# Optimization experiments

Measured on AMD Instinct MI355X. Metric: run time of the kernel, lower is better.

The kernel has to match this reference:

```python
import jax, jax.numpy as jnp
import numpy as np

D_MODEL = 1024
NUM_HEADS = 16
D_K = D_MODEL // NUM_HEADS
EPS = 1e-6


def setup_inputs() -> dict:
    key = jax.random.key(0)
    ks = jax.random.split(key, 16)
    B, S = 2, 2048
    sc_in = 1.0 / np.sqrt(D_MODEL)
    sc_na = 1.0 / np.sqrt(D_K)
    inp = {
        "Q": jax.random.normal(ks[0], (B, S, D_MODEL), jnp.float32),
        "K": jax.random.normal(ks[1], (B, S, D_MODEL), jnp.float32),
        "V": jax.random.normal(ks[2], (B, S, D_MODEL), jnp.float32),
        "mask": jax.random.randint(ks[3], (1, 1, S, S), 0, 2, jnp.int32),
        # projection weights stored [in, out] (math-equivalent to torch Linear)
        "wq": jax.random.normal(ks[4], (D_MODEL, D_MODEL), jnp.float32) * sc_in,
        "bq": jnp.zeros((D_MODEL,), jnp.float32),
        "wk": jax.random.normal(ks[5], (D_MODEL, D_MODEL), jnp.float32) * sc_in,
        "bk": jnp.zeros((D_MODEL,), jnp.float32),
        "wv": jax.random.normal(ks[6], (D_MODEL, D_MODEL), jnp.float32) * sc_in,
        "bv": jnp.zeros((D_MODEL,), jnp.float32),
        "wo": jax.random.normal(ks[7], (D_MODEL, D_MODEL), jnp.float32) * sc_in,
        "bo": jnp.zeros((D_MODEL,), jnp.float32),
        # NeuralAttention score-fn params (per-head-dim transforms)
        "wnq": jax.random.normal(ks[8], (D_K, D_K), jnp.float32) * sc_na,
        "bnq": jnp.zeros((D_K,), jnp.float32),
        "wnk": jax.random.normal(ks[9], (D_K, D_K), jnp.float32) * sc_na,
        "bnk": jnp.zeros((D_K,), jnp.float32),
        "temperature": jnp.ones((NUM_HEADS, 1, 1), jnp.float32),
        "gamma": jnp.ones((D_MODEL,), jnp.float32),
    }
    return inp


def _split_heads(x):
    B, S, _ = x.shape
    return x.reshape(B, S, NUM_HEADS, D_K).transpose(0, 2, 1, 3)  # [B,H,S,dk]


def reference(Q, K, V, mask, wq, bq, wk, bk, wv, bv, wo, bo,
              wnq, bnq, wnk, bnk, temperature, gamma):
    B, S, _ = Q.shape
    q = _split_heads(Q @ wq + bq)  # [B,H,S,dk]
    k = _split_heads(K @ wk + bk)
    v = _split_heads(V @ wv + bv)
    # NeuralAttention: nonlinear per-token feature maps, then contraction
    qf = jnp.tanh(q @ wnq + bnq)
    kf = jnp.tanh(k @ wnk + bnk)
    scores = jnp.einsum('bhqd,bhkd->bhqk', qf, kf) / jnp.sqrt(jnp.float32(D_K))
    scores = scores / temperature  # [H,1,1] broadcasts over [B,H,S,S]
    scores = jnp.where(mask == 0, jnp.float32(-1e9), scores)
    attn = jax.nn.softmax(scores, axis=-1)
    ctx = jnp.einsum('bhqk,bhkd->bhqd', attn, v)
    out = ctx.transpose(0, 2, 1, 3).reshape(B, S, D_MODEL) @ wo + bo
    # RMSNorm
    rms = jax.lax.rsqrt(jnp.mean(out * out, axis=-1, keepdims=True) + EPS)
    return out * rms * gamma
```

## Files before the change

kernel.cpp:

```cpp
#include <hip/hip_runtime.h>
#include <hip/hip_bf16.h>
#include <math.h>

#define S_LEN 2048
#define BATCH 2
#define NH 16
#define DK 64
#define DM 1024
#define BS (BATCH * S_LEN)
#define BHS (BATCH * NH * S_LEN)
#define TRP 72
#define PSTR 72

using bf16x8  = __attribute__((ext_vector_type(8))) __bf16;
using floatx4 = __attribute__((ext_vector_type(4))) float;
using ushort4v = __attribute__((ext_vector_type(4))) unsigned short;

extern "C" __device__ float __ocml_exp2_f32(float);

__device__ __forceinline__ unsigned short f2bf(float f) {
    union { float f; unsigned u; } v; v.f = f;
    unsigned r = v.u + 0x7fffu + ((v.u >> 16) & 1u);
    return (unsigned short)(r >> 16);
}

__device__ __forceinline__ unsigned cvt_pk_bf16(float a, float b) {
    unsigned r;
    asm("v_cvt_pk_bf16_f32 %0, %1, %2" : "=v"(r) : "v"(a), "v"(b));
    return r;
}

__device__ __forceinline__ float fast_tanh(float x) {
    float e = __ocml_exp2_f32(x * 2.8853900817779268f);
    return 1.0f - 2.0f / (e + 1.0f);
}

__device__ __forceinline__ void gl2lds16(const void* g, void* l) {
    __builtin_amdgcn_global_load_lds(
        (__attribute__((address_space(1))) void*)(uintptr_t)g,
        (__attribute__((address_space(3))) void*)(uintptr_t)l,
        16, 0, 0);
}

__global__ void k_convert(const float* __restrict__ q, const float* __restrict__ k,
                          const float* __restrict__ v,
                          unsigned short* __restrict__ qb, unsigned short* __restrict__ kb,
                          unsigned short* __restrict__ vb) {
    const int N4 = BS * DM / 4;
    int i = blockIdx.x * 256 + threadIdx.x;
    int which = i / N4;
    int off = i - which * N4;
    const floatx4* src = (const floatx4*)(which == 0 ? q : which == 1 ? k : v);
    unsigned short* dst = which == 0 ? qb : which == 1 ? kb : vb;
    floatx4 x = src[off];
    ushort4v o;
    unsigned p01 = cvt_pk_bf16(x[0], x[1]);
    unsigned p23 = cvt_pk_bf16(x[2], x[3]);
    o[0] = (unsigned short)p01; o[1] = (unsigned short)(p01 >> 16);
    o[2] = (unsigned short)p23; o[3] = (unsigned short)(p23 >> 16);
    ((ushort4v*)dst)[off] = o;
}

__global__ void k_transpose(const float* s0, const float* s1, const float* s2, const float* s3,
                            unsigned short* d0, unsigned short* d1, unsigned short* d2,
                            unsigned short* d3, int n) {
    int z = blockIdx.z;
    const float* src = z == 0 ? s0 : z == 1 ? s1 : z == 2 ? s2 : s3;
    unsigned short* dst = z == 0 ? d0 : z == 1 ? d1 : z == 2 ? d2 : d3;
    __shared__ unsigned short tile[32][33];
    int tx = threadIdx.x & 31, ty = threadIdx.x >> 5;
#pragma unroll
    for (int i = 0; i < 4; i++) {
        int y = blockIdx.y * 32 + i * 8 + ty;
        tile[i * 8 + ty][tx] = f2bf(src[(size_t)y * n + blockIdx.x * 32 + tx]);
    }
    __syncthreads();
#pragma unroll
    for (int i = 0; i < 4; i++) {
        int r = blockIdx.x * 32 + i * 8 + ty;
        dst[(size_t)r * n + blockIdx.y * 32 + tx] = tile[tx][i * 8 + ty];
    }
}

__global__ void k_maskpack(const int* __restrict__ mask, unsigned int* __restrict__ mb) {
    int t = blockIdx.x * 256 + threadIdx.x;
    int row = t >> 6, w = t & 63;
    const int* p = mask + (size_t)row * S_LEN + w * 32;
    unsigned bits = 0;
#pragma unroll
    for (int i = 0; i < 32; i++) bits |= (p[i] != 0 ? 1u : 0u) << i;
    mb[t] = bits;
}

__global__ __launch_bounds__(256) void k_gemm_qkv(
    const unsigned short* __restrict__ Qb, const unsigned short* __restrict__ Kb,
    const unsigned short* __restrict__ Vb,
    const unsigned short* __restrict__ Wqt, const unsigned short* __restrict__ Wkt,
    const unsigned short* __restrict__ Wvt,
    const float* __restrict__ bq, const float* __restrict__ bk, const float* __restrict__ bv,
    const unsigned short* __restrict__ wnqt, const unsigned short* __restrict__ wnkt,
    const float* __restrict__ bnq, const float* __restrict__ bnk,
    const float* __restrict__ temp,
    unsigned short* __restrict__ qfb, unsigned short* __restrict__ kfrag,
    unsigned short* __restrict__ vfrag) {
    const int K = DM;
    int z = blockIdx.z;
    const unsigned short* A  = z == 0 ? Qb  : z == 1 ? Kb  : Vb;
    const unsigned short* Wt = z == 0 ? Wqt : z == 1 ? Wkt : Wvt;
    const float* bias        = z == 0 ? bq  : z == 1 ? bk  : bv;
    int m0 = blockIdx.y * 128, n0 = blockIdx.x * 128;
    __shared__ unsigned short As[128 * 32];
    __shared__ unsigned short Bs[128 * 32];
    __shared__ unsigned short Tr[4][32 * TRP];
    int tid = threadIdx.x;
    int lane = tid & 63, wid = tid >> 6;
    int wy = wid >> 1, wx = wid & 1;
    int l16 = lane & 15, quad = lane >> 4;

    floatx4 acc[4][4] = {};

    for (int kt = 0; kt < K / 32; kt++) {
        int kk = kt * 32;
#pragma unroll
        for (int i = 0; i < 2; i++) {
            int c = i * 256 + tid;
            int row = c >> 2, seg = c & 3;
            gl2lds16(A + (size_t)(m0 + row) * K + kk + seg * 8, &As[c * 8]);
            gl2lds16(Wt + (size_t)(n0 + row) * K + kk + seg * 8, &Bs[c * 8]);
        }
        __syncthreads();
        bf16x8 af[4], bf[4];
#pragma unroll
        for (int mi = 0; mi < 4; mi++)
            af[mi] = *(const bf16x8*)&As[(wy * 64 + mi * 16 + l16) * 32 + quad * 8];
#pragma unroll
        for (int ni = 0; ni < 4; ni++)
            bf[ni] = *(const bf16x8*)&Bs[(wx * 64 + ni * 16 + l16) * 32 + quad * 8];
#pragma unroll
        for (int mi = 0; mi < 4; mi++)
#pragma unroll
            for (int ni = 0; ni < 4; ni++)
                acc[mi][ni] = __builtin_amdgcn_mfma_f32_16x16x32_bf16(af[mi], bf[ni], acc[mi][ni], 0, 0, 0);
        __syncthreads();
    }

    float bvv[4];
#pragma unroll
    for (int ni = 0; ni < 4; ni++) bvv[ni] = bias[n0 + wx * 64 + ni * 16 + l16];
    int head = (n0 + wx * 64) >> 6;
    int mbase = m0 + wy * 64;
    int b = mbase >> 11;
    int bh = b * NH + head;
    unsigned short* tw = &Tr[wid][0];

    if (z == 2) {
        int kt2 = (mbase & (S_LEN - 1)) >> 6;
        size_t tilebase = ((size_t)bh * 32 + kt2) * 4096;
#pragma unroll
        for (int hh = 0; hh < 2; hh++) {
#pragma unroll
            for (int ni2 = 0; ni2 < 2; ni2++) {
                int ni = hh * 2 + ni2;
#pragma unroll
                for (int mi = 0; mi < 4; mi++) {
                    unsigned p01 = cvt_pk_bf16(acc[mi][ni][0] + bvv[ni], acc[mi][ni][1] + bvv[ni]);
                    unsigned p23 = cvt_pk_bf16(acc[mi][ni][2] + bvv[ni], acc[mi][ni][3] + bvv[ni]);
                    int ad = (ni2 * 16 + l16) * TRP + mi * 16 + quad * 4;
                    *(unsigned*)&tw[ad] = p01;
                    *(unsigned*)&tw[ad + 2] = p23;
                }
            }
#pragma unroll
            for (int c = 0; c < 4; c++) {
                int ad = ((c >> 1) * 16 + l16) * TRP + (c & 1) * 32 + quad * 8;
                bf16x8 vv = *(const bf16x8*)&tw[ad];
                *(bf16x8*)&vfrag[tilebase + (size_t)(4 * hh + c) * 512 + lane * 8] = vv;
            }
        }
    } else {
        const unsigned short* wn = z == 0 ? wnqt : wnkt;
        const float* bn = z == 0 ? bnq : bnk;
        float sc = z == 0 ? 1.4426950408889634f / (8.0f * temp[head]) : 1.0f;
        bf16x8 wf[4][2];
        float bnv[4];
#pragma unroll
        for (int ni = 0; ni < 4; ni++) {
            bnv[ni] = bn[ni * 16 + l16];
#pragma unroll
            for (int ks = 0; ks < 2; ks++)
                wf[ni][ks] = *(const bf16x8*)(wn + (size_t)(ni * 16 + l16) * DK + ks * 32 + quad * 8);
        }
        size_t rowbase = (size_t)((size_t)bh * S_LEN + (mbase & (S_LEN - 1))) * DK;
        int kt2 = (mbase & (S_LEN - 1)) >> 6;
        size_t tb = ((size_t)bh * 32 + kt2) * 4096;
#pragma unroll
        for (int hh = 0; hh < 2; hh++) {
#pragma unroll
            for (int mi2 = 0; mi2 < 2; mi2++) {
                int mi = hh * 2 + mi2;
#pragma unroll
                for (int ni = 0; ni < 4; ni++) {
                    unsigned p01 = cvt_pk_bf16(acc[mi][ni][0] + bvv[ni], acc[mi][ni][1] + bvv[ni]);
                    unsigned p23 = cvt_pk_bf16(acc[mi][ni][2] + bvv[ni], acc[mi][ni][3] + bvv[ni]);
                    int ad = (mi2 * 16 + quad * 4) * TRP + ni * 16 + l16;
                    tw[ad] = (unsigned short)p01;
                    tw[ad + TRP] = (unsigned short)(p01 >> 16);
                    tw[ad + 2 * TRP] = (unsigned short)p23;
                    tw[ad + 3 * TRP] = (unsigned short)(p23 >> 16);
                }
            }
            floatx4 facc[2][4] = {};
#pragma unroll
            for (int mg = 0; mg < 2; mg++) {
                bf16x8 af2[2];
#pragma unroll
                for (int ks = 0; ks < 2; ks++)
                    af2[ks] = *(const bf16x8*)&tw[(mg * 16 + l16) * TRP + ks * 32 + quad * 8];
#pragma unroll
                for (int ni = 0; ni < 4; ni++) {
                    facc[mg][ni] = __builtin_amdgcn_mfma_f32_16x16x32_bf16(af2[0], wf[ni][0], facc[mg][ni], 0, 0, 0);
                    facc[mg][ni] = __builtin_amdgcn_mfma_f32_16x16x32_bf16(af2[1], wf[ni][1], facc[mg][ni], 0, 0, 0);
                }
            }
#pragma unroll
            for (int mg = 0; mg < 2; mg++) {
#pragma unroll
                for (int ni = 0; ni < 4; ni++) {
                    float t0 = fast_tanh(facc[mg][ni][0] + bnv[ni]) * sc;
                    float t1 = fast_tanh(facc[mg][ni][1] + bnv[ni]) * sc;
                    float t2 = fast_tanh(facc[mg][ni][2] + bnv[ni]) * sc;
                    float t3 = fast_tanh(facc[mg][ni][3] + bnv[ni]) * sc;
                    unsigned p01 = cvt_pk_bf16(t0, t1);
                    unsigned p23 = cvt_pk_bf16(t2, t3);
                    int ad = (mg * 16 + quad * 4) * TRP + ni * 16 + l16;
                    tw[ad] = (unsigned short)p01;
                    tw[ad + TRP] = (unsigned short)(p01 >> 16);
                    tw[ad + 2 * TRP] = (unsigned short)p23;
                    tw[ad + 3 * TRP] = (unsigned short)(p23 >> 16);
                }
            }
            if (z == 0) {
#pragma unroll
                for (int c = 0; c < 4; c++) {
                    int g = c * 64 + lane;
                    int ml = g >> 3, dc = g & 7;
                    bf16x8 vv = *(const bf16x8*)&tw[ml * TRP + dc * 8];
                    *(bf16x8*)&qfb[rowbase + (size_t)(hh * 32 + ml) * DK + dc * 8] = vv;
                }
            } else {
#pragma unroll
                for (int c = 0; c < 4; c++) {
                    int ad = ((c >> 1) * 16 + l16) * TRP + (c & 1) * 32 + quad * 8;
                    bf16x8 vv = *(const bf16x8*)&tw[ad];
                    *(bf16x8*)&kfrag[tb + (size_t)(hh * 4 + c) * 512 + lane * 8] = vv;
                }
            }
        }
    }
}

__global__ __launch_bounds__(256) void k_gemm_out(const unsigned short* __restrict__ A,
                                                  const unsigned short* __restrict__ Wt,
                                                  const float* __restrict__ bias,
                                                  float* __restrict__ out_f32) {
    const int K = DM;
    int m0 = blockIdx.y * 128, n0 = blockIdx.x * 128;
    __shared__ unsigned short As[128 * 32];
    __shared__ unsigned short Bs[128 * 32];
    int tid = threadIdx.x;
    int lane = tid & 63, wid = tid >> 6;
    int wy = wid >> 1, wx = wid & 1;
    int l16 = lane & 15, quad = lane >> 4;

    floatx4 acc[4][4] = {};

    for (int kt = 0; kt < K / 32; kt++) {
        int kk = kt * 32;
#pragma unroll
        for (int i = 0; i < 2; i++) {
            int c = i * 256 + tid;
            int row = c >> 2, seg = c & 3;
            gl2lds16(A + (size_t)(m0 + row) * K + kk + seg * 8, &As[c * 8]);
            gl2lds16(Wt + (size_t)(n0 + row) * K + kk + seg * 8, &Bs[c * 8]);
        }
        __syncthreads();
        bf16x8 af[4], bf[4];
#pragma unroll
        for (int mi = 0; mi < 4; mi++)
            af[mi] = *(const bf16x8*)&As[(wy * 64 + mi * 16 + l16) * 32 + quad * 8];
#pragma unroll
        for (int ni = 0; ni < 4; ni++)
            bf[ni] = *(const bf16x8*)&Bs[(wx * 64 + ni * 16 + l16) * 32 + quad * 8];
#pragma unroll
        for (int mi = 0; mi < 4; mi++)
#pragma unroll
            for (int ni = 0; ni < 4; ni++)
                acc[mi][ni] = __builtin_amdgcn_mfma_f32_16x16x32_bf16(af[mi], bf[ni], acc[mi][ni], 0, 0, 0);
        __syncthreads();
    }

#pragma unroll
    for (int mi = 0; mi < 4; mi++) {
#pragma unroll
        for (int ni = 0; ni < 4; ni++) {
            int col = n0 + wx * 64 + ni * 16 + l16;
            float bvv = bias[col];
#pragma unroll
            for (int r = 0; r < 4; r++) {
                int row = m0 + wy * 64 + mi * 16 + quad * 4 + r;
                out_f32[(size_t)row * DM + col] = acc[mi][ni][r] + bvv;
            }
        }
    }
}

__global__ __launch_bounds__(256, 2) void k_attn(const unsigned short* __restrict__ qf,
                                                 const unsigned short* __restrict__ kfr,
                                                 const unsigned short* __restrict__ vfr,
                                                 const unsigned long long* __restrict__ mb64,
                                                 unsigned short* __restrict__ ctx) {
    int tid = threadIdx.x, lane = tid & 63, wid = tid >> 6;
    int l16 = lane & 15, quad = lane >> 4;
    int bh = blockIdx.y;
    int b = bh >> 4, h = bh & 15;
    int q0 = blockIdx.x * 128 + wid * 32;

    const unsigned short* qfb = qf + (size_t)bh * S_LEN * DK;
    const unsigned short* kbase = kfr + (size_t)bh * 32 * 4096;
    const unsigned short* vbase = vfr + (size_t)bh * 32 * 4096;

    __shared__ unsigned short Kbuf[2][4096];
    __shared__ unsigned short Plds[4][32 * PSTR];
    unsigned short* myP = Plds[wid];

    bf16x8 bq[2][2];
#pragma unroll
    for (int g = 0; g < 2; g++)
#pragma unroll
        for (int ks = 0; ks < 2; ks++)
            bq[g][ks] = *(const bf16x8*)(qfb + (size_t)(q0 + g * 16 + l16) * DK + ks * 32 + quad * 8);

    gl2lds16(kbase + tid * 8, &Kbuf[0][tid * 8]);
    gl2lds16(kbase + 2048 + tid * 8, &Kbuf[0][2048 + tid * 8]);

    floatx4 oacc[2][4] = {};
    float lrow[2] = {0.f, 0.f};
    const unsigned long long* mq0 = mb64 + (size_t)(q0 + l16) * 32;
    const unsigned long long* mq1 = mb64 + (size_t)(q0 + 16 + l16) * 32;

    for (int kt = 0; kt < S_LEN / 64; kt++) {
        __syncthreads();
        int nb = (kt + 1) & 1;
        const unsigned short* kn = kbase + (size_t)((kt + 1) & 31) * 4096;
        gl2lds16(kn + tid * 8, &Kbuf[nb][tid * 8]);
        gl2lds16(kn + 2048 + tid * 8, &Kbuf[nb][2048 + tid * 8]);
        const unsigned short* vt = vbase + (size_t)kt * 4096 + lane * 8;
        bf16x8 vf[8];
#pragma unroll
        for (int i = 0; i < 8; i++) vf[i] = *(const bf16x8*)(vt + i * 512);
        unsigned long long mw[2] = {mq0[kt], mq1[kt]};
        const unsigned short* kb = &Kbuf[kt & 1][lane * 8];
        bf16x8 kf8[8];
#pragma unroll
        for (int i = 0; i < 8; i++) kf8[i] = *(const bf16x8*)(kb + i * 512);
#pragma unroll
        for (int g = 0; g < 2; g++) {
            unsigned short* pw = myP + (g * 16 + l16) * PSTR;
#pragma unroll
            for (int kbk = 0; kbk < 4; kbk++) {
                floatx4 s = {};
                s = __builtin_amdgcn_mfma_f32_16x16x32_bf16(kf8[kbk * 2], bq[g][0], s, 0, 0, 0);
                s = __builtin_amdgcn_mfma_f32_16x16x32_bf16(kf8[kbk * 2 + 1], bq[g][1], s, 0, 0, 0);
                unsigned w = (unsigned)(mw[g] >> (kbk * 16 + quad * 4));
                float p0 = __ocml_exp2_f32((w & 1u) ? s[0] : -23.0f);
                float p1 = __ocml_exp2_f32((w & 2u) ? s[1] : -23.0f);
                float p2 = __ocml_exp2_f32((w & 4u) ? s[2] : -23.0f);
                float p3 = __ocml_exp2_f32((w & 8u) ? s[3] : -23.0f);
                lrow[g] += (p0 + p1) + (p2 + p3);
                *(unsigned*)&pw[kbk * 16 + quad * 4] = cvt_pk_bf16(p0, p1);
                *(unsigned*)&pw[kbk * 16 + quad * 4 + 2] = cvt_pk_bf16(p2, p3);
            }
            bf16x8 pa0 = *(const bf16x8*)&myP[(g * 16 + l16) * PSTR + quad * 8];
            bf16x8 pa1 = *(const bf16x8*)&myP[(g * 16 + l16) * PSTR + 32 + quad * 8];
#pragma unroll
            for (int ni = 0; ni < 4; ni++) {
                oacc[g][ni] = __builtin_amdgcn_mfma_f32_16x16x32_bf16(pa0, vf[ni * 2], oacc[g][ni], 0, 0, 0);
                oacc[g][ni] = __builtin_amdgcn_mfma_f32_16x16x32_bf16(pa1, vf[ni * 2 + 1], oacc[g][ni], 0, 0, 0);
            }
        }
    }
#pragma unroll
    for (int g = 0; g < 2; g++) {
        float lr = lrow[g];
        lr += __shfl_xor(lr, 16);
        lr += __shfl_xor(lr, 32);
        float inv[4];
#pragma unroll
        for (int r = 0; r < 4; r++) inv[r] = 1.0f / __shfl(lr, quad * 4 + r, 16);
#pragma unroll
        for (int ni = 0; ni < 4; ni++) {
            int d = ni * 16 + l16;
#pragma unroll
            for (int r = 0; r < 4; r++) {
                int s = q0 + g * 16 + quad * 4 + r;
                ctx[(size_t)(b * S_LEN + s) * DM + h * DK + d] = f2bf(oacc[g][ni][r] * inv[r]);
            }
        }
    }
}

__global__ __launch_bounds__(256) void k_rmsnorm(const float* __restrict__ x,
                                                 const float* __restrict__ gamma,
                                                 float* __restrict__ out) {
    int row = blockIdx.x, tid = threadIdx.x;
    const floatx4* xr = (const floatx4*)(x + (size_t)row * DM);
    floatx4 v = xr[tid];
    float ss = v[0] * v[0] + v[1] * v[1] + v[2] * v[2] + v[3] * v[3];
#pragma unroll
    for (int off = 1; off < 64; off <<= 1) ss += __shfl_xor(ss, off);
    __shared__ float red[4];
    int lane = tid & 63, wid = tid >> 6;
    if (lane == 0) red[wid] = ss;
    __syncthreads();
    float tot = red[0] + red[1] + red[2] + red[3];
    float rms = rsqrtf(tot * (1.0f / DM) + 1e-6f);
    floatx4 g = ((const floatx4*)gamma)[tid];
    floatx4 o;
    o[0] = v[0] * rms * g[0];
    o[1] = v[1] * rms * g[1];
    o[2] = v[2] * rms * g[2];
    o[3] = v[3] * rms * g[3];
    ((floatx4*)(out + (size_t)row * DM))[tid] = o;
}

extern "C" void kernel_launch(void* const* d_in, const int* in_sizes, int n_in,
                              void* d_out, int out_size, void* d_ws, size_t ws_size,
                              hipStream_t stream) {
    const float* Q = (const float*)d_in[0];
    const float* K = (const float*)d_in[1];
    const float* V = (const float*)d_in[2];
    const int* mask = (const int*)d_in[3];
    const float* wq = (const float*)d_in[4];
    const float* bq = (const float*)d_in[5];
    const float* wk = (const float*)d_in[6];
    const float* bk = (const float*)d_in[7];
    const float* wv = (const float*)d_in[8];
    const float* bv = (const float*)d_in[9];
    const float* wo = (const float*)d_in[10];
    const float* bo = (const float*)d_in[11];
    const float* wnq = (const float*)d_in[12];
    const float* bnq = (const float*)d_in[13];
    const float* wnk = (const float*)d_in[14];
    const float* bnk = (const float*)d_in[15];
    const float* temp = (const float*)d_in[16];
    const float* gamma = (const float*)d_in[17];

    char* w = (char*)d_ws;
    size_t o = 0;
    auto alloc = [&](size_t bytes) {
        char* p = w + o;
        o += (bytes + 255) & ~(size_t)255;
        return p;
    };
    unsigned short* Qb = (unsigned short*)alloc((size_t)BS * DM * 2);
    unsigned short* Kb = (unsigned short*)alloc((size_t)BS * DM * 2);
    unsigned short* Vb = (unsigned short*)alloc((size_t)BS * DM * 2);
    unsigned short* Wqt = (unsigned short*)alloc((size_t)DM * DM * 2);
    unsigned short* Wkt = (unsigned short*)alloc((size_t)DM * DM * 2);
    unsigned short* Wvt = (unsigned short*)alloc((size_t)DM * DM * 2);
    unsigned short* Wot = (unsigned short*)alloc((size_t)DM * DM * 2);
    unsigned short* wnqt = (unsigned short*)alloc((size_t)DK * DK * 2);
    unsigned short* wnkt = (unsigned short*)alloc((size_t)DK * DK * 2);
    unsigned short* vfrag = (unsigned short*)alloc((size_t)BHS * DK * 2);
    unsigned short* qfb = (unsigned short*)alloc((size_t)BHS * DK * 2);
    unsigned short* kfrag = (unsigned short*)alloc((size_t)BHS * DK * 2);
    unsigned int* mb = (unsigned int*)alloc((size_t)S_LEN * (S_LEN / 32) * 4);
    unsigned short* ctx = (unsigned short*)alloc((size_t)BS * DM * 2);
    float* outt = (float*)alloc((size_t)BS * DM * 4);

    k_convert<<<dim3(3 * BS * DM / 4 / 256), 256, 0, stream>>>(Q, K, V, Qb, Kb, Vb);
    k_transpose<<<dim3(32, 32, 4), 256, 0, stream>>>(wq, wk, wv, wo, Wqt, Wkt, Wvt, Wot, DM);
    k_transpose<<<dim3(2, 2, 2), 256, 0, stream>>>(wnq, wnk, wnq, wnq, wnqt, wnkt, wnqt, wnqt, DK);
    k_maskpack<<<dim3(S_LEN * 64 / 256), 256, 0, stream>>>(mask, mb);

    k_gemm_qkv<<<dim3(8, 32, 3), 256, 0, stream>>>(Qb, Kb, Vb, Wqt, Wkt, Wvt,
                                                   bq, bk, bv, wnqt, wnkt, bnq, bnk, temp,
                                                   qfb, kfrag, vfrag);

    k_attn<<<dim3(S_LEN / 128, BATCH * NH), 256, 0, stream>>>(
        qfb, kfrag, vfrag, (const unsigned long long*)mb, ctx);

    k_gemm_out<<<dim3(8, 32), 256, 0, stream>>>(ctx, Wot, bo, outt);
    k_rmsnorm<<<dim3(BS), 256, 0, stream>>>(outt, gamma, (float*)d_out);
}
```

Before: 303.3 us.

## Split attention over key range, combine partials, and shrink output GEMM tiles

Result: slower. 325.8 us (+7.4%).

```diff
diff --git a/kernel.cpp b/kernel.cpp
--- a/kernel.cpp
+++ b/kernel.cpp
@@ -264,35 +264,33 @@
                                                   const float* __restrict__ bias,
                                                   float* __restrict__ out_f32) {
     const int K = DM;
-    int m0 = blockIdx.y * 128, n0 = blockIdx.x * 128;
+    int m0 = blockIdx.y * 128, n0 = blockIdx.x * 64;
     __shared__ unsigned short As[128 * 32];
-    __shared__ unsigned short Bs[128 * 32];
+    __shared__ unsigned short Bs[64 * 32];
     int tid = threadIdx.x;
     int lane = tid & 63, wid = tid >> 6;
-    int wy = wid >> 1, wx = wid & 1;
     int l16 = lane & 15, quad = lane >> 4;
 
-    floatx4 acc[4][4] = {};
+    floatx4 acc[2][4] = {};
 
     for (int kt = 0; kt < K / 32; kt++) {
         int kk = kt * 32;
 #pragma unroll
         for (int i = 0; i < 2; i++) {
             int c = i * 256 + tid;
-            int row = c >> 2, seg = c & 3;
-            gl2lds16(A + (size_t)(m0 + row) * K + kk + seg * 8, &As[c * 8]);
-            gl2lds16(Wt + (size_t)(n0 + row) * K + kk + seg * 8, &Bs[c * 8]);
-        }
+            gl2lds16(A + (size_t)(m0 + (c >> 2)) * K + kk + (c & 3) * 8, &As[c * 8]);
+        }
+        gl2lds16(Wt + (size_t)(n0 + (tid >> 2)) * K + kk + (tid & 3) * 8, &Bs[tid * 8]);
         __syncthreads();
-        bf16x8 af[4], bf[4];
-#pragma unroll
-        for (int mi = 0; mi < 4; mi++)
-            af[mi] = *(const bf16x8*)&As[(wy * 64 + mi * 16 + l16) * 32 + quad * 8];
+        bf16x8 af[2], bf[4];
+#pragma unroll
+        for (int mi = 0; mi < 2; mi++)
+            af[mi] = *(const bf16x8*)&As[(wid * 32 + mi * 16 + l16) * 32 + quad * 8];
 #pragma unroll
         for (int ni = 0; ni < 4; ni++)
-            bf[ni] = *(const bf16x8*)&Bs[(wx * 64 + ni * 16 + l16) * 32 + quad * 8];
-#pragma unroll
-        for (int mi = 0; mi < 4; mi++)
+            bf[ni] = *(const bf16x8*)&Bs[(ni * 16 + l16) * 32 + quad * 8];
+#pragma unroll
+        for (int mi = 0; mi < 2; mi++)
 #pragma unroll
             for (int ni = 0; ni < 4; ni++)
                 acc[mi][ni] = __builtin_amdgcn_mfma_f32_16x16x32_bf16(af[mi], bf[ni], acc[mi][ni], 0, 0, 0);
@@ -300,30 +298,32 @@
     }
 
 #pragma unroll
-    for (int mi = 0; mi < 4; mi++) {
+    for (int mi = 0; mi < 2; mi++) {
 #pragma unroll
         for (int ni = 0; ni < 4; ni++) {
-            int col = n0 + wx * 64 + ni * 16 + l16;
+            int col = n0 + ni * 16 + l16;
             float bvv = bias[col];
 #pragma unroll
             for (int r = 0; r < 4; r++) {
-                int row = m0 + wy * 64 + mi * 16 + quad * 4 + r;
+                int row = m0 + wid * 32 + mi * 16 + quad * 4 + r;
                 out_f32[(size_t)row * DM + col] = acc[mi][ni][r] + bvv;
             }
         }
     }
 }
 
-__global__ __launch_bounds__(256, 2) void k_attn(const unsigned short* __restrict__ qf,
+__global__ __launch_bounds__(256, 4) void k_attn(const unsigned short* __restrict__ qf,
                                                  const unsigned short* __restrict__ kfr,
                                                  const unsigned short* __restrict__ vfr,
                                                  const unsigned long long* __restrict__ mb64,
-                                                 unsigned short* __restrict__ ctx) {
+                                                 float* __restrict__ Opart,
+                                                 float* __restrict__ Lpart) {
     int tid = threadIdx.x, lane = tid & 63, wid = tid >> 6;
     int l16 = lane & 15, quad = lane >> 4;
     int bh = blockIdx.y;
-    int b = bh >> 4, h = bh & 15;
+    int z = blockIdx.z;
     int q0 = blockIdx.x * 128 + wid * 32;
+    int kt0 = z * 16;
 
     const unsigned short* qfb = qf + (size_t)bh * S_LEN * DK;
     const unsigned short* kbase = kfr + (size_t)bh * 32 * 4096;
@@ -333,6 +333,11 @@
     __shared__ unsigned short Plds[4][32 * PSTR];
     unsigned short* myP = Plds[wid];
 
+    union { bf16x8 v; unsigned short u[8]; } one_u;
+#pragma unroll
+    for (int j = 0; j < 8; j++) one_u.u[j] = 0x3F80;
+    bf16x8 ones = one_u.v;
+
     bf16x8 bq[2][2];
 #pragma unroll
     for (int g = 0; g < 2; g++)
@@ -340,18 +345,19 @@
         for (int ks = 0; ks < 2; ks++)
             bq[g][ks] = *(const bf16x8*)(qfb + (size_t)(q0 + g * 16 + l16) * DK + ks * 32 + quad * 8);
 
-    gl2lds16(kbase + tid * 8, &Kbuf[0][tid * 8]);
-    gl2lds16(kbase + 2048 + tid * 8, &Kbuf[0][2048 + tid * 8]);
+    gl2lds16(kbase + (size_t)kt0 * 4096 + tid * 8, &Kbuf[0][tid * 8]);
+    gl2lds16(kbase + (size_t)kt0 * 4096 + 2048 + tid * 8, &Kbuf[0][2048 + tid * 8]);
 
     floatx4 oacc[2][4] = {};
-    float lrow[2] = {0.f, 0.f};
+    floatx4 lacc[2] = {};
     const unsigned long long* mq0 = mb64 + (size_t)(q0 + l16) * 32;
     const unsigned long long* mq1 = mb64 + (size_t)(q0 + 16 + l16) * 32;
 
-    for (int kt = 0; kt < S_LEN / 64; kt++) {
+    for (int lk = 0; lk < 16; lk++) {
+        int kt = kt0 + lk;
         __syncthreads();
-        int nb = (kt + 1) & 1;
-        const unsigned short* kn = kbase + (size_t)((kt + 1) & 31) * 4096;
+        int nb = (lk + 1) & 1;
+        const unsigned short* kn = kbase + (size_t)(kt0 + ((lk + 1) & 15)) * 4096;
         gl2lds16(kn + tid * 8, &Kbuf[nb][tid * 8]);
         gl2lds16(kn + 2048 + tid * 8, &Kbuf[nb][2048 + tid * 8]);
         const unsigned short* vt = vbase + (size_t)kt * 4096 + lane * 8;
@@ -359,7 +365,7 @@
 #pragma unroll
         for (int i = 0; i < 8; i++) vf[i] = *(const bf16x8*)(vt + i * 512);
         unsigned long long mw[2] = {mq0[kt], mq1[kt]};
-        const unsigned short* kb = &Kbuf[kt & 1][lane * 8];
+        const unsigned short* kb = &Kbuf[lk & 1][lane * 8];
         bf16x8 kf8[8];
 #pragma unroll
         for (int i = 0; i < 8; i++) kf8[i] = *(const bf16x8*)(kb + i * 512);
@@ -376,12 +382,13 @@
                 float p1 = __ocml_exp2_f32((w & 2u) ? s[1] : -23.0f);
                 float p2 = __ocml_exp2_f32((w & 4u) ? s[2] : -23.0f);
                 float p3 = __ocml_exp2_f32((w & 8u) ? s[3] : -23.0f);
-                lrow[g] += (p0 + p1) + (p2 + p3);
                 *(unsigned*)&pw[kbk * 16 + quad * 4] = cvt_pk_bf16(p0, p1);
                 *(unsigned*)&pw[kbk * 16 + quad * 4 + 2] = cvt_pk_bf16(p2, p3);
             }
             bf16x8 pa0 = *(const bf16x8*)&myP[(g * 16 + l16) * PSTR + quad * 8];
             bf16x8 pa1 = *(const bf16x8*)&myP[(g * 16 + l16) * PSTR + 32 + quad * 8];
+            lacc[g] = __builtin_amdgcn_mfma_f32_16x16x32_bf16(pa0, ones, lacc[g], 0, 0, 0);
+            lacc[g] = __builtin_amdgcn_mfma_f32_16x16x32_bf16(pa1, ones, lacc[g], 0, 0, 0);
 #pragma unroll
             for (int ni = 0; ni < 4; ni++) {
                 oacc[g][ni] = __builtin_amdgcn_mfma_f32_16x16x32_bf16(pa0, vf[ni * 2], oacc[g][ni], 0, 0, 0);
@@ -389,24 +396,42 @@
             }
         }
     }
+    size_t obase = ((size_t)z * BHS + (size_t)bh * S_LEN) * DK;
+    size_t lbase = (size_t)z * BHS + (size_t)bh * S_LEN;
 #pragma unroll
     for (int g = 0; g < 2; g++) {
-        float lr = lrow[g];
-        lr += __shfl_xor(lr, 16);
-        lr += __shfl_xor(lr, 32);
-        float inv[4];
-#pragma unroll
-        for (int r = 0; r < 4; r++) inv[r] = 1.0f / __shfl(lr, quad * 4 + r, 16);
+        if (l16 == 0) {
+#pragma unroll
+            for (int r = 0; r < 4; r++)
+                Lpart[lbase + q0 + g * 16 + quad * 4 + r] = lacc[g][r];
+        }
 #pragma unroll
         for (int ni = 0; ni < 4; ni++) {
-            int d = ni * 16 + l16;
-#pragma unroll
-            for (int r = 0; r < 4; r++) {
-                int s = q0 + g * 16 + quad * 4 + r;
-                ctx[(size_t)(b * S_LEN + s) * DM + h * DK + d] = f2bf(oacc[g][ni][r] * inv[r]);
-            }
-        }
-    }
+#pragma unroll
+            for (int r = 0; r < 4; r++)
+                Opart[obase + (size_t)(q0 + g * 16 + quad * 4 + r) * DK + ni * 16 + l16] = oacc[g][ni][r];
+        }
+    }
+}
+
+__global__ __launch_bounds__(256) void k_combine(const float* __restrict__ O,
+                                                 const float* __restrict__ L,
+                                                 unsigned short* __restrict__ ctx) {
+    int gid = blockIdx.x * 256 + threadIdx.x;
+    size_t flat = (size_t)gid * 4;
+    int row = gid >> 4;
+    int d0 = (gid & 15) * 4;
+    floatx4 o0 = *(const floatx4*)&O[flat];
+    floatx4 o1 = *(const floatx4*)&O[(size_t)BHS * DK + flat];
+    float ri = 1.0f / (L[row] + L[BHS + row]);
+    int bh = row >> 11, s = row & (S_LEN - 1);
+    int b = bh >> 4, h = bh & 15;
+    unsigned p01 = cvt_pk_bf16((o0[0] + o1[0]) * ri, (o0[1] + o1[1]) * ri);
+    unsigned p23 = cvt_pk_bf16((o0[2] + o1[2]) * ri, (o0[3] + o1[3]) * ri);
+    ushort4v o;
+    o[0] = (unsigned short)p01; o[1] = (unsigned short)(p01 >> 16);
+    o[2] = (unsigned short)p23; o[3] = (unsigned short)(p23 >> 16);
+    *(ushort4v*)&ctx[((size_t)(b * S_LEN + s)) * DM + h * DK + d0] = o;
 }
 
 __global__ __launch_bounds__(256) void k_rmsnorm(const float* __restrict__ x,
@@ -477,6 +502,8 @@
     unsigned int* mb = (unsigned int*)alloc((size_t)S_LEN * (S_LEN / 32) * 4);
     unsigned short* ctx = (unsigned short*)alloc((size_t)BS * DM * 2);
     float* outt = (float*)alloc((size_t)BS * DM * 4);
+    float* Opart = (float*)alloc((size_t)2 * BHS * DK * 4);
+    float* Lpart = (float*)alloc((size_t)2 * BHS * 4);
 
     k_convert<<<dim3(3 * BS * DM / 4 / 256), 256, 0, stream>>>(Q, K, V, Qb, Kb, Vb);
     k_transpose<<<dim3(32, 32, 4), 256, 0, stream>>>(wq, wk, wv, wo, Wqt, Wkt, Wvt, Wot, DM);
@@ -487,9 +514,11 @@
                                                    bq, bk, bv, wnqt, wnkt, bnq, bnk, temp,
                                                    qfb, kfrag, vfrag);
 
-    k_attn<<<dim3(S_LEN / 128, BATCH * NH), 256, 0, stream>>>(
-        qfb, kfrag, vfrag, (const unsigned long long*)mb, ctx);
-
-    k_gemm_out<<<dim3(8, 32), 256, 0, stream>>>(ctx, Wot, bo, outt);
+    k_attn<<<dim3(S_LEN / 128, BATCH * NH, 2), 256, 0, stream>>>(
+        qfb, kfrag, vfrag, (const unsigned long long*)mb, Opart, Lpart);
+
+    k_combine<<<dim3(BHS * DK / 4 / 256), 256, 0, stream>>>(Opart, Lpart, ctx);
+
+    k_gemm_out<<<dim3(16, 32), 256, 0, stream>>>(ctx, Wot, bo, outt);
     k_rmsnorm<<<dim3(BS), 256, 0, stream>>>(outt, gamma, (float*)d_out);
 }
```

## Shrink attention and output-GEMM tiles for more blocks; MFMA row sums

Applied to the files above, without the earlier changes.

New measurement: 298.7 us. About the same (-1.5%).

```diff
diff --git a/kernel.cpp b/kernel.cpp
--- a/kernel.cpp
+++ b/kernel.cpp
@@ -264,35 +264,33 @@
                                                   const float* __restrict__ bias,
                                                   float* __restrict__ out_f32) {
     const int K = DM;
-    int m0 = blockIdx.y * 128, n0 = blockIdx.x * 128;
+    int m0 = blockIdx.y * 128, n0 = blockIdx.x * 64;
     __shared__ unsigned short As[128 * 32];
-    __shared__ unsigned short Bs[128 * 32];
+    __shared__ unsigned short Bs[64 * 32];
     int tid = threadIdx.x;
     int lane = tid & 63, wid = tid >> 6;
-    int wy = wid >> 1, wx = wid & 1;
     int l16 = lane & 15, quad = lane >> 4;
 
-    floatx4 acc[4][4] = {};
+    floatx4 acc[2][4] = {};
 
     for (int kt = 0; kt < K / 32; kt++) {
         int kk = kt * 32;
 #pragma unroll
         for (int i = 0; i < 2; i++) {
             int c = i * 256 + tid;
-            int row = c >> 2, seg = c & 3;
-            gl2lds16(A + (size_t)(m0 + row) * K + kk + seg * 8, &As[c * 8]);
-            gl2lds16(Wt + (size_t)(n0 + row) * K + kk + seg * 8, &Bs[c * 8]);
-        }
+            gl2lds16(A + (size_t)(m0 + (c >> 2)) * K + kk + (c & 3) * 8, &As[c * 8]);
+        }
+        gl2lds16(Wt + (size_t)(n0 + (tid >> 2)) * K + kk + (tid & 3) * 8, &Bs[tid * 8]);
         __syncthreads();
-        bf16x8 af[4], bf[4];
-#pragma unroll
-        for (int mi = 0; mi < 4; mi++)
-            af[mi] = *(const bf16x8*)&As[(wy * 64 + mi * 16 + l16) * 32 + quad * 8];
+        bf16x8 af[2], bf[4];
+#pragma unroll
+        for (int mi = 0; mi < 2; mi++)
+            af[mi] = *(const bf16x8*)&As[(wid * 32 + mi * 16 + l16) * 32 + quad * 8];
 #pragma unroll
         for (int ni = 0; ni < 4; ni++)
-            bf[ni] = *(const bf16x8*)&Bs[(wx * 64 + ni * 16 + l16) * 32 + quad * 8];
-#pragma unroll
-        for (int mi = 0; mi < 4; mi++)
+            bf[ni] = *(const bf16x8*)&Bs[(ni * 16 + l16) * 32 + quad * 8];
+#pragma unroll
+        for (int mi = 0; mi < 2; mi++)
 #pragma unroll
             for (int ni = 0; ni < 4; ni++)
                 acc[mi][ni] = __builtin_amdgcn_mfma_f32_16x16x32_bf16(af[mi], bf[ni], acc[mi][ni], 0, 0, 0);
@@ -300,21 +298,21 @@
     }
 
 #pragma unroll
-    for (int mi = 0; mi < 4; mi++) {
+    for (int mi = 0; mi < 2; mi++) {
 #pragma unroll
         for (int ni = 0; ni < 4; ni++) {
-            int col = n0 + wx * 64 + ni * 16 + l16;
+            int col = n0 + ni * 16 + l16;
             float bvv = bias[col];
 #pragma unroll
             for (int r = 0; r < 4; r++) {
-                int row = m0 + wy * 64 + mi * 16 + quad * 4 + r;
+                int row = m0 + wid * 32 + mi * 16 + quad * 4 + r;
                 out_f32[(size_t)row * DM + col] = acc[mi][ni][r] + bvv;
             }
         }
     }
 }
 
-__global__ __launch_bounds__(256, 2) void k_attn(const unsigned short* __restrict__ qf,
+__global__ __launch_bounds__(256, 4) void k_attn(const unsigned short* __restrict__ qf,
                                                  const unsigned short* __restrict__ kfr,
                                                  const unsigned short* __restrict__ vfr,
                                                  const unsigned long long* __restrict__ mb64,
@@ -323,32 +321,34 @@
     int l16 = lane & 15, quad = lane >> 4;
     int bh = blockIdx.y;
     int b = bh >> 4, h = bh & 15;
-    int q0 = blockIdx.x * 128 + wid * 32;
+    int q0 = blockIdx.x * 64 + wid * 16;
 
     const unsigned short* qfb = qf + (size_t)bh * S_LEN * DK;
     const unsigned short* kbase = kfr + (size_t)bh * 32 * 4096;
     const unsigned short* vbase = vfr + (size_t)bh * 32 * 4096;
 
     __shared__ unsigned short Kbuf[2][4096];
-    __shared__ unsigned short Plds[4][32 * PSTR];
+    __shared__ unsigned short Plds[4][16 * PSTR];
     unsigned short* myP = Plds[wid];
 
-    bf16x8 bq[2][2];
-#pragma unroll
-    for (int g = 0; g < 2; g++)
-#pragma unroll
-        for (int ks = 0; ks < 2; ks++)
-            bq[g][ks] = *(const bf16x8*)(qfb + (size_t)(q0 + g * 16 + l16) * DK + ks * 32 + quad * 8);
+    union { bf16x8 v; unsigned short u[8]; } one_u;
+#pragma unroll
+    for (int j = 0; j < 8; j++) one_u.u[j] = 0x3F80;
+    bf16x8 ones = one_u.v;
+
+    bf16x8 bq[2];
+#pragma unroll
+    for (int ks = 0; ks < 2; ks++)
+        bq[ks] = *(const bf16x8*)(qfb + (size_t)(q0 + l16) * DK + ks * 32 + quad * 8);
 
     gl2lds16(kbase + tid * 8, &Kbuf[0][tid * 8]);
     gl2lds16(kbase + 2048 + tid * 8, &Kbuf[0][2048 + tid * 8]);
 
-    floatx4 oacc[2][4] = {};
-    float lrow[2] = {0.f, 0.f};
-    const unsigned long long* mq0 = mb64 + (size_t)(q0 + l16) * 32;
-    const unsigned long long* mq1 = mb64 + (size_t)(q0 + 16 + l16) * 32;
-
-    for (int kt = 0; kt < S_LEN / 64; kt++) {
+    floatx4 oacc[4] = {};
+    floatx4 lacc = {};
+    const unsigned long long* mq = mb64 + (size_t)(q0 + l16) * 32;
+
+    for (int kt = 0; kt < 32; kt++) {
         __syncthreads();
         int nb = (kt + 1) & 1;
         const unsigned short* kn = kbase + (size_t)((kt + 1) & 31) * 4096;
@@ -358,53 +358,45 @@
         bf16x8 vf[8];
 #pragma unroll
         for (int i = 0; i < 8; i++) vf[i] = *(const bf16x8*)(vt + i * 512);
-        unsigned long long mw[2] = {mq0[kt], mq1[kt]};
+        unsigned long long mw = mq[kt];
         const unsigned short* kb = &Kbuf[kt & 1][lane * 8];
         bf16x8 kf8[8];
 #pragma unroll
         for (int i = 0; i < 8; i++) kf8[i] = *(const bf16x8*)(kb + i * 512);
-#pragma unroll
-        for (int g = 0; g < 2; g++) {
-            unsigned short* pw = myP + (g * 16 + l16) * PSTR;
-#pragma unroll
-            for (int kbk = 0; kbk < 4; kbk++) {
-                floatx4 s = {};
-                s = __builtin_amdgcn_mfma_f32_16x16x32_bf16(kf8[kbk * 2], bq[g][0], s, 0, 0, 0);
-                s = __builtin_amdgcn_mfma_f32_16x16x32_bf16(kf8[kbk * 2 + 1], bq[g][1], s, 0, 0, 0);
-                unsigned w = (unsigned)(mw[g] >> (kbk * 16 + quad * 4));
-                float p0 = __ocml_exp2_f32((w & 1u) ? s[0] : -23.0f);
-                float p1 = __ocml_exp2_f32((w & 2u) ? s[1] : -23.0f);
-                float p2 = __ocml_exp2_f32((w & 4u) ? s[2] : -23.0f);
-                float p3 = __ocml_exp2_f32((w & 8u) ? s[3] : -23.0f);
-                lrow[g] += (p0 + p1) + (p2 + p3);
-                *(unsigned*)&pw[kbk * 16 + quad * 4] = cvt_pk_bf16(p0, p1);
-                *(unsigned*)&pw[kbk * 16 + quad * 4 + 2] = cvt_pk_bf16(p2, p3);
-            }
-            bf16x8 pa0 = *(const bf16x8*)&myP[(g * 16 + l16) * PSTR + quad * 8];
-            bf16x8 pa1 = *(const bf16x8*)&myP[(g * 16 + l16) * PSTR + 32 + quad * 8];
-#pragma unroll
-            for (int ni = 0; ni < 4; ni++) {
-                oacc[g][ni] = __builtin_amdgcn_mfma_f32_16x16x32_bf16(pa0, vf[ni * 2], oacc[g][ni], 0, 0, 0);
-                oacc[g][ni] = __builtin_amdgcn_mfma_f32_16x16x32_bf16(pa1, vf[ni * 2 + 1], oacc[g][ni], 0, 0, 0);
-            }
-        }
-    }
-#pragma unroll
-    for (int g = 0; g < 2; g++) {
-        float lr = lrow[g];
-        lr += __shfl_xor(lr, 16);
-        lr += __shfl_xor(lr, 32);
-        float inv[4];
-#pragma unroll
-        for (int r = 0; r < 4; r++) inv[r] = 1.0f / __shfl(lr, quad * 4 + r, 16);
+        unsigned short* pw = myP + l16 * PSTR;
+#pragma unroll
+        for (int kbk = 0; kbk < 4; kbk++) {
+            floatx4 s = {};
+            s = __builtin_amdgcn_mfma_f32_16x16x32_bf16(kf8[kbk * 2], bq[0], s, 0, 0, 0);
+            s = __builtin_amdgcn_mfma_f32_16x16x32_bf16(kf8[kbk * 2 + 1], bq[1], s, 0, 0, 0);
+            unsigned w = (unsigned)(mw >> (kbk * 16 + quad * 4));
+            float p0 = __ocml_exp2_f32((w & 1u) ? s[0] : -23.0f);
+            float p1 = __ocml_exp2_f32((w & 2u) ? s[1] : -23.0f);
+            float p2 = __ocml_exp2_f32((w & 4u) ? s[2] : -23.0f);
+            float p3 = __ocml_exp2_f32((w & 8u) ? s[3] : -23.0f);
+            *(unsigned*)&pw[kbk * 16 + quad * 4] = cvt_pk_bf16(p0, p1);
+            *(unsigned*)&pw[kbk * 16 + quad * 4 + 2] = cvt_pk_bf16(p2, p3);
+        }
+        bf16x8 pa0 = *(const bf16x8*)&myP[l16 * PSTR + quad * 8];
+        bf16x8 pa1 = *(const bf16x8*)&myP[l16 * PSTR + 32 + quad * 8];
+        lacc = __builtin_amdgcn_mfma_f32_16x16x32_bf16(pa0, ones, lacc, 0, 0, 0);
+        lacc = __builtin_amdgcn_mfma_f32_16x16x32_bf16(pa1, ones, lacc, 0, 0, 0);
 #pragma unroll
         for (int ni = 0; ni < 4; ni++) {
-            int d = ni * 16 + l16;
-#pragma unroll
-            for (int r = 0; r < 4; r++) {
-                int s = q0 + g * 16 + quad * 4 + r;
-                ctx[(size_t)(b * S_LEN + s) * DM + h * DK + d] = f2bf(oacc[g][ni][r] * inv[r]);
-            }
+            oacc[ni] = __builtin_amdgcn_mfma_f32_16x16x32_bf16(pa0, vf[ni * 2], oacc[ni], 0, 0, 0);
+            oacc[ni] = __builtin_amdgcn_mfma_f32_16x16x32_bf16(pa1, vf[ni * 2 + 1], oacc[ni], 0, 0, 0);
+        }
+    }
+    float inv[4];
+#pragma unroll
+    for (int r = 0; r < 4; r++) inv[r] = 1.0f / lacc[r];
+#pragma unroll
+    for (int ni = 0; ni < 4; ni++) {
+        int d = ni * 16 + l16;
+#pragma unroll
+        for (int r = 0; r < 4; r++) {
+            int s = q0 + quad * 4 + r;
+            ctx[(size_t)(b * S_LEN + s) * DM + h * DK + d] = f2bf(oacc[ni][r] * inv[r]);
         }
     }
 }
@@ -487,9 +479,9 @@
                                                    bq, bk, bv, wnqt, wnkt, bnq, bnk, temp,
                                                    qfb, kfrag, vfrag);
 
-    k_attn<<<dim3(S_LEN / 128, BATCH * NH), 256, 0, stream>>>(
+    k_attn<<<dim3(S_LEN / 64, BATCH * NH), 256, 0, stream>>>(
         qfb, kfrag, vfrag, (const unsigned long long*)mb, ctx);
 
-    k_gemm_out<<<dim3(8, 32), 256, 0, stream>>>(ctx, Wot, bo, outt);
+    k_gemm_out<<<dim3(16, 32), 256, 0, stream>>>(ctx, Wot, bo, outt);
     k_rmsnorm<<<dim3(BS), 256, 0, stream>>>(outt, gamma, (float*)d_out);
 }
```
